# Optimization experiments

Measured on AMD Instinct MI355X. Metric: run time of the kernel, lower is better.

## Reference

```python
import jax, jax.numpy as jnp
import numpy as np

B, T, D_EMB, D_QKV = 8, 2048, 1024, 64
SCALE = 1.0 / (D_QKV ** 0.5)


def setup_inputs() -> dict:
    key = jax.random.key(0)
    kx, kq, kk, kv = jax.random.split(key, 4)
    return {
        "x": jax.random.normal(kx, (B, T, D_EMB), dtype=jnp.float32),
        "Wq": jax.random.normal(kq, (D_EMB, D_QKV), dtype=jnp.float32) * 0.02,
        "Wk": jax.random.normal(kk, (D_EMB, D_QKV), dtype=jnp.float32) * 0.02,
        "Wv": jax.random.normal(kv, (D_EMB, D_QKV), dtype=jnp.float32) * 0.02,
    }


def reference(x, Wq, Wk, Wv):
    # x: [B, T, D_emb]; projections to [B, T, D_qkv]
    q = jnp.einsum("bte,ed->btd", x, Wq)
    k = jnp.einsum("bte,ed->btd", x, Wk)
    v = jnp.einsum("bte,ed->btd", x, Wv)
    # scores: [B, T, T], scaled then causally masked
    scores = jnp.einsum("bqd,bkd->bqk", q, k) * SCALE
    t = x.shape[1]
    causal = jnp.tril(jnp.ones((t, t), dtype=bool))
    scores = jnp.where(causal[None, :, :], scores, -jnp.inf)
    attn = jax.nn.softmax(scores, axis=-1)
    return jnp.einsum("bqk,bkd->bqd", attn, v)
```

## Files before the change

kernel.cpp:

```cpp
#include <hip/hip_runtime.h>

typedef float f32x4 __attribute__((ext_vector_type(4)));
typedef __bf16 bf16x8 __attribute__((ext_vector_type(8)));
typedef __bf16 bf16x4 __attribute__((ext_vector_type(4)));

#define T_ 2048
#define DE 1024
#define DQ 64
#define SCALE 0.125f

#define GL16(gp, lp)                                                        \
  __builtin_amdgcn_global_load_lds(                                         \
      (const __attribute__((address_space(1))) void*)(gp),                  \
      (__attribute__((address_space(3))) void*)(lp), 16, 0, 0)

#define WAITVM(N) asm volatile("s_waitcnt vmcnt(" #N ")" ::: "memory")

__global__ __launch_bounds__(256) void kw_pack(
    const float* __restrict__ Wq, const float* __restrict__ Wk,
    const float* __restrict__ Wv, __bf16* __restrict__ Wf)
{
  int tid = blockIdx.x * 256 + threadIdx.x;
  int lane = tid & 63, f = tid >> 6;
  int t = f % 12, kc = f / 12;
  const float* W = (t < 4) ? Wq : ((t < 8) ? Wk : Wv);
  int nl = (t & 3) * 16 + (lane & 15);
  int k0 = kc * 32 + (lane >> 4) * 8;
  bf16x8 v;
#pragma unroll
  for (int j = 0; j < 8; ++j) v[j] = (__bf16)W[(size_t)(k0 + j) * 64 + nl];
  *(bf16x8*)(Wf + (size_t)tid * 8) = v;
}

__global__ __launch_bounds__(256) void kproj(
    const float* __restrict__ x, const __bf16* __restrict__ Wf,
    __bf16* __restrict__ Qb, __bf16* __restrict__ Kb, __bf16* __restrict__ Vt)
{
  __shared__ char lds[3 * 8192 + 2 * 24576];
  const int tid = threadIdx.x;
  const int lane = tid & 63;
  const int w = tid >> 6;
  const int col = lane & 15, g = lane >> 4;
  const int msub = w & 1;
  const int ng = w >> 1;
  const int mbase = blockIdx.x * 32;

  size_t gsrcA[2];
  int ldstA[2];
#pragma unroll
  for (int cc = 0; cc < 2; ++cc) {
    int q = w * 2 + cc;
    int row = q * 4 + (lane >> 4);
    int kbyte = ((lane & 15) * 16) ^ ((row & 7) << 4);
    gsrcA[cc] = (size_t)(mbase + row) * 4096 + (size_t)kbyte;
    ldstA[cc] = q * 1024 + lane * 16;
  }
  int ofsB[6];
#pragma unroll
  for (int cc = 0; cc < 6; ++cc) ofsB[cc] = (w * 6 + cc) * 1024 + lane * 16;

  f32x4 acc[6];
#pragma unroll
  for (int i = 0; i < 6; ++i) acc[i] = (f32x4){0.f, 0.f, 0.f, 0.f};

  const char* xb = (const char*)x;
  const char* wb = (const char*)Wf;

#define STAGE_A(ks)                                                         \
  {                                                                         \
    char* lb = &lds[((ks) % 3) * 8192];                                     \
    _Pragma("unroll")                                                       \
    for (int cc = 0; cc < 2; ++cc)                                          \
      GL16(xb + gsrcA[cc] + (size_t)(ks) * 256, lb + ldstA[cc]);            \
  }
#define STAGE_B(ks)                                                         \
  {                                                                         \
    char* lb = &lds[24576 + ((ks) & 1) * 24576];                            \
    _Pragma("unroll")                                                       \
    for (int cc = 0; cc < 6; ++cc)                                          \
      GL16(wb + (size_t)(ks) * 24576 + ofsB[cc], lb + ofsB[cc]);            \
  }
#define KSTEP(ks)                                                           \
  {                                                                         \
    const char* la = &lds[((ks) % 3) * 8192];                               \
    const char* lbB = &lds[24576 + ((ks) & 1) * 24576];                     \
    const int arow = msub * 16 + col;                                       \
    const char* abase = la + arow * 256;                                    \
    const int sw = (arow & 7) << 4;                                         \
    _Pragma("unroll")                                                       \
    for (int kh = 0; kh < 2; ++kh) {                                        \
      int kb = kh * 128 + g * 32;                                           \
      f32x4 a0 = *(const f32x4*)(abase + (kb ^ sw));                        \
      f32x4 a1 = *(const f32x4*)(abase + ((kb + 16) ^ sw));                 \
      bf16x8 af;                                                            \
      _Pragma("unroll")                                                     \
      for (int j = 0; j < 4; ++j) { af[j] = (__bf16)a0[j]; af[4 + j] = (__bf16)a1[j]; } \
      _Pragma("unroll")                                                     \
      for (int ii = 0; ii < 6; ++ii) {                                      \
        int nt = ng * 6 + ii;                                               \
        bf16x8 bfr = *(const bf16x8*)(lbB + ((kh * 12 + nt) * 64 + lane) * 16); \
        acc[ii] = __builtin_amdgcn_mfma_f32_16x16x32_bf16(af, bfr, acc[ii], 0, 0, 0); \
      }                                                                     \
    }                                                                       \
  }
#define ITER(ks, vm, doB, doA)                                              \
  WAITVM(vm);                                                               \
  __builtin_amdgcn_s_barrier();                                             \
  __builtin_amdgcn_sched_barrier(0);                                        \
  if (doB) STAGE_B((ks) + 1);                                               \
  if (doA) STAGE_A((ks) + 2);                                               \
  KSTEP(ks);

  STAGE_A(0);
  STAGE_B(0);
  STAGE_A(1);

  ITER(0, 2, 1, 1)  ITER(1, 2, 1, 1)  ITER(2, 2, 1, 1)  ITER(3, 2, 1, 1)
  ITER(4, 2, 1, 1)  ITER(5, 2, 1, 1)  ITER(6, 2, 1, 1)  ITER(7, 2, 1, 1)
  ITER(8, 2, 1, 1)  ITER(9, 2, 1, 1)  ITER(10, 2, 1, 1) ITER(11, 2, 1, 1)
  ITER(12, 2, 1, 1) ITER(13, 2, 1, 1) ITER(14, 2, 1, 0) ITER(15, 0, 0, 0)

#undef ITER
#undef KSTEP
#undef STAGE_B
#undef STAGE_A

  const int b = mbase >> 11;
  const int mrow = mbase + msub * 16 + g * 4;
  const int trow = (mbase & 2047) + msub * 16 + g * 4;
#pragma unroll
  for (int ii = 0; ii < 6; ++ii) {
    int ti = ng * 6 + ii;
    if (ti < 8) {
      __bf16* dst = (ti < 4) ? Qb : Kb;
      int c = (ti & 3) * 16 + col;
#pragma unroll
      for (int r = 0; r < 4; ++r)
        dst[(size_t)(mrow + r) * DQ + c] = (__bf16)acc[ii][r];
    } else {
      int d = (ti - 8) * 16 + col;
      bf16x4 v;
#pragma unroll
      for (int r = 0; r < 4; ++r) v[r] = (__bf16)acc[ii][r];
      *(bf16x4*)(Vt + ((size_t)(b * DQ + d)) * T_ + trow) = v;
    }
  }
}

__global__ __launch_bounds__(256) void kattn(
    const __bf16* __restrict__ Qb, const __bf16* __restrict__ Kb,
    const __bf16* __restrict__ Vt, float* __restrict__ out)
{
  __shared__ char smem[84992];
  const int tid = threadIdx.x;
  const int lane = tid & 63;
  const int w = tid >> 6;
  const int col = lane & 15, g = lane >> 4;
  const int b = blockIdx.x & 7;
  const int jq = 63 - (blockIdx.x >> 3);
  const int qbase = jq * 32;

  char* kbuf = smem + w * 16384;
  char* vbuf = kbuf + 8192;
  __bf16* pld = (__bf16*)(smem + 65536 + w * 4608);
  float* mls = (float*)(smem + 83968);

  bf16x8 qa[2][2];
#pragma unroll
  for (int mt = 0; mt < 2; ++mt) {
    const __bf16* Qp = Qb + (size_t)(b * T_ + qbase + mt * 16 + col) * DQ + g * 8;
    qa[mt][0] = *(const bf16x8*)(Qp);
    qa[mt][1] = *(const bf16x8*)(Qp + 32);
  }

  const char* Kbb = (const char*)(Kb + (size_t)b * T_ * DQ);
  const char* Vbb = (const char*)(Vt + (size_t)b * DQ * T_);

  size_t gofK[8], gofV[8];
  int lof[8];
#pragma unroll
  for (int c = 0; c < 8; ++c) {
    int o = (c * 64 + lane) * 16;
    int row = o >> 7, slot = (o >> 4) & 7;
    int sl = (slot * 16) ^ ((row & 7) << 4);
    lof[c] = o;
    gofK[c] = (size_t)row * 128 + sl;
    gofV[c] = (size_t)row * 4096 + sl;
  }

  f32x4 acc[2][4];
#pragma unroll
  for (int mt = 0; mt < 2; ++mt)
#pragma unroll
    for (int dt = 0; dt < 4; ++dt) acc[mt][dt] = (f32x4){0.f,0.f,0.f,0.f};
  float mrun[2][4], lsum[2][4];
#pragma unroll
  for (int mt = 0; mt < 2; ++mt)
#pragma unroll
    for (int r = 0; r < 4; ++r) { mrun[mt][r] = -1e30f; lsum[mt][r] = 0.f; }

  const int nb = (jq >> 1) + 1;

  if (w < nb) {
    const char* ksrc = Kbb + (size_t)(w * 64) * 128;
    const char* vsrc = Vbb + (size_t)(w * 64) * 2;
#pragma unroll
    for (int c = 0; c < 8; ++c) GL16(ksrc + gofK[c], kbuf + lof[c]);
#pragma unroll
    for (int c = 0; c < 8; ++c) GL16(vsrc + gofV[c], vbuf + lof[c]);
  }

  for (int it = w; it < nb; it += 4) {
    const int nbase = it * 64;

    WAITVM(0);
    __builtin_amdgcn_sched_barrier(0);

    bf16x8 kf_[4][2], vf[4][2];
#pragma unroll
    for (int nt = 0; nt < 4; ++nt)
#pragma unroll
      for (int h = 0; h < 2; ++h) {
        int krow = nt * 16 + col;
        int bo = krow * 128 + ((h * 64 + g * 16) ^ ((krow & 7) << 4));
        kf_[nt][h] = *(const bf16x8*)(kbuf + bo);
        vf[nt][h]  = *(const bf16x8*)(vbuf + bo);
      }
    asm volatile("s_waitcnt lgkmcnt(0)" ::: "memory");
    __builtin_amdgcn_sched_barrier(0);

    if (it + 4 < nb) {
      const char* ksrc = Kbb + (size_t)((it + 4) * 64) * 128;
      const char* vsrc = Vbb + (size_t)((it + 4) * 64) * 2;
#pragma unroll
      for (int c = 0; c < 8; ++c) GL16(ksrc + gofK[c], kbuf + lof[c]);
#pragma unroll
      for (int c = 0; c < 8; ++c) GL16(vsrc + gofV[c], vbuf + lof[c]);
    }
    __builtin_amdgcn_sched_barrier(0);

    f32x4 s[2][4];
#pragma unroll
    for (int mt = 0; mt < 2; ++mt)
#pragma unroll
      for (int nt = 0; nt < 4; ++nt) {
        f32x4 t = __builtin_amdgcn_mfma_f32_16x16x32_bf16(qa[mt][0], kf_[nt][0],
                                                          (f32x4){0.f,0.f,0.f,0.f}, 0, 0, 0);
        s[mt][nt] = __builtin_amdgcn_mfma_f32_16x16x32_bf16(qa[mt][1], kf_[nt][1], t, 0, 0, 0);
      }

#pragma unroll
    for (int mt = 0; mt < 2; ++mt)
#pragma unroll
      for (int nt = 0; nt < 4; ++nt)
#pragma unroll
        for (int r = 0; r < 4; ++r) s[mt][nt][r] *= SCALE;
    if (it == nb - 1) {
#pragma unroll
      for (int mt = 0; mt < 2; ++mt)
#pragma unroll
        for (int nt = 0; nt < 4; ++nt)
#pragma unroll
          for (int r = 0; r < 4; ++r)
            if (nbase + nt * 16 + col > qbase + mt * 16 + g * 4 + r) s[mt][nt][r] = -1e30f;
    }

    float pmax[2][4];
#pragma unroll
    for (int mt = 0; mt < 2; ++mt)
#pragma unroll
      for (int r = 0; r < 4; ++r)
        pmax[mt][r] = fmaxf(fmaxf(s[mt][0][r], s[mt][1][r]), fmaxf(s[mt][2][r], s[mt][3][r]));
    bool need = false;
#pragma unroll
    for (int mt = 0; mt < 2; ++mt)
#pragma unroll
      for (int r = 0; r < 4; ++r)
        need = need || (pmax[mt][r] > mrun[mt][r] + 8.f);

    if (__any(need)) {
      float mv[2][4];
#pragma unroll
      for (int mt = 0; mt < 2; ++mt)
#pragma unroll
        for (int r = 0; r < 4; ++r) mv[mt][r] = pmax[mt][r];
#pragma unroll
      for (int sh = 1; sh <= 8; sh <<= 1)
#pragma unroll
        for (int mt = 0; mt < 2; ++mt)
#pragma unroll
          for (int r = 0; r < 4; ++r) mv[mt][r] = fmaxf(mv[mt][r], __shfl_xor(mv[mt][r], sh, 64));
#pragma unroll
      for (int mt = 0; mt < 2; ++mt)
#pragma unroll
        for (int r = 0; r < 4; ++r) {
          float mn = fmaxf(mrun[mt][r], mv[mt][r]);
          float rs = __expf(mrun[mt][r] - mn);
          mrun[mt][r] = mn;
          float ps = 0.f;
#pragma unroll
          for (int nt = 0; nt < 4; ++nt) {
            s[mt][nt][r] = __expf(s[mt][nt][r] - mn);
            ps += s[mt][nt][r];
          }
          lsum[mt][r] = lsum[mt][r] * rs + ps;
#pragma unroll
          for (int dt = 0; dt < 4; ++dt) acc[mt][dt][r] *= rs;
        }
    } else {
#pragma unroll
      for (int mt = 0; mt < 2; ++mt)
#pragma unroll
        for (int r = 0; r < 4; ++r) {
          float ps = 0.f;
#pragma unroll
          for (int nt = 0; nt < 4; ++nt) {
            s[mt][nt][r] = __expf(s[mt][nt][r] - mrun[mt][r]);
            ps += s[mt][nt][r];
          }
          lsum[mt][r] += ps;
        }
    }

#pragma unroll
    for (int mt = 0; mt < 2; ++mt)
#pragma unroll
      for (int nt = 0; nt < 4; ++nt)
#pragma unroll
        for (int r = 0; r < 4; ++r)
          pld[(mt * 16 + g * 4 + r) * 72 + nt * 16 + col] = (__bf16)s[mt][nt][r];

    bf16x8 pa[2][2];
#pragma unroll
    for (int mt = 0; mt < 2; ++mt) {
      pa[mt][0] = *(const bf16x8*)&pld[(mt * 16 + col) * 72 + g * 8];
      pa[mt][1] = *(const bf16x8*)&pld[(mt * 16 + col) * 72 + 32 + g * 8];
    }

#pragma unroll
    for (int mt = 0; mt < 2; ++mt)
#pragma unroll
      for (int dt = 0; dt < 4; ++dt) {
        f32x4 t = __builtin_amdgcn_mfma_f32_16x16x32_bf16(pa[mt][0], vf[dt][0], acc[mt][dt], 0, 0, 0);
        acc[mt][dt] = __builtin_amdgcn_mfma_f32_16x16x32_bf16(pa[mt][1], vf[dt][1], t, 0, 0, 0);
      }
  }

#pragma unroll
  for (int sh = 1; sh <= 8; sh <<= 1)
#pragma unroll
    for (int mt = 0; mt < 2; ++mt)
#pragma unroll
      for (int r = 0; r < 4; ++r) lsum[mt][r] += __shfl_xor(lsum[mt][r], sh, 64);

  float* accw = (float*)(smem + w * 16384);
#pragma unroll
  for (int mt = 0; mt < 2; ++mt)
#pragma unroll
    for (int r = 0; r < 4; ++r) {
      int row = mt * 16 + g * 4 + r;
      accw[row * 68 + col]      = acc[mt][0][r];
      accw[row * 68 + col + 16] = acc[mt][1][r];
      accw[row * 68 + col + 32] = acc[mt][2][r];
      accw[row * 68 + col + 48] = acc[mt][3][r];
      if (col == 0) { mls[(w * 2 + 0) * 32 + row] = mrun[mt][r]; mls[(w * 2 + 1) * 32 + row] = lsum[mt][r]; }
    }
  __syncthreads();

#pragma unroll
  for (int pass = 0; pass < 2; ++pass) {
    int row = pass * 16 + (tid >> 4);
    int c4 = (tid & 15) * 4;
    float m0 = mls[0 * 32 + row], m1 = mls[2 * 32 + row];
    float m2 = mls[4 * 32 + row], m3 = mls[6 * 32 + row];
    float M = fmaxf(fmaxf(m0, m1), fmaxf(m2, m3));
    float s0 = __expf(m0 - M), s1 = __expf(m1 - M);
    float s2 = __expf(m2 - M), s3 = __expf(m3 - M);
    float L = s0 * mls[1 * 32 + row] + s1 * mls[3 * 32 + row]
            + s2 * mls[5 * 32 + row] + s3 * mls[7 * 32 + row];
    f32x4 a0 = *(const f32x4*)((float*)(smem + 0 * 16384) + row * 68 + c4);
    f32x4 a1 = *(const f32x4*)((float*)(smem + 1 * 16384) + row * 68 + c4);
    f32x4 a2 = *(const f32x4*)((float*)(smem + 2 * 16384) + row * 68 + c4);
    f32x4 a3 = *(const f32x4*)((float*)(smem + 3 * 16384) + row * 68 + c4);
    float inv = 1.f / L;
    f32x4 o;
#pragma unroll
    for (int j = 0; j < 4; ++j)
      o[j] = (s0 * a0[j] + s1 * a1[j] + s2 * a2[j] + s3 * a3[j]) * inv;
    *(f32x4*)(out + (size_t)(b * T_ + qbase + row) * DQ + c4) = o;
  }
}

extern "C" void kernel_launch(void* const* d_in, const int* in_sizes, int n_in,
                              void* d_out, int out_size, void* d_ws, size_t ws_size,
                              hipStream_t stream)
{
  const float* x  = (const float*)d_in[0];
  const float* Wq = (const float*)d_in[1];
  const float* Wk = (const float*)d_in[2];
  const float* Wv = (const float*)d_in[3];
  float* out = (float*)d_out;

  char* ws = (char*)d_ws;
  __bf16* Wf = (__bf16*)(ws);
  __bf16* Qb = (__bf16*)(ws + 0x80000);
  __bf16* Kb = (__bf16*)(ws + 0x80000 + 0x200000);
  __bf16* Vt = (__bf16*)(ws + 0x80000 + 0x400000);

  kw_pack<<<96, 256, 0, stream>>>(Wq, Wk, Wv, Wf);
  kproj<<<512, 256, 0, stream>>>(x, Wf, Qb, Kb, Vt);
  kattn<<<512, 256, 0, stream>>>(Qb, Kb, Vt, out);
}
```

Measured before the change: 46.86 us.

## Enlarge projection tile to 64 rows and reuse weight fragments across four M-fragments

The projection kernel now handles 64 rows of x per block instead of 32, and each wave owns 3 of the 12 output N-tiles across all four 16-row M-fragments. Each B fragment loaded from LDS is reused for four MFMAs, and the whole-block weight staging is amortised over twice as many rows. The cost is a grid of 256 blocks instead of 512 on a 256-CU part, more accumulator registers, a larger LDS footprint (~96KB) that limits occupancy, and deeper outstanding-load waits.

```diff
diff --git a/kernel.cpp b/kernel.cpp
--- a/kernel.cpp
+++ b/kernel.cpp
@@ -36,20 +36,19 @@
     const float* __restrict__ x, const __bf16* __restrict__ Wf,
     __bf16* __restrict__ Qb, __bf16* __restrict__ Kb, __bf16* __restrict__ Vt)
 {
-  __shared__ char lds[3 * 8192 + 2 * 24576];
+  __shared__ char lds[3 * 16384 + 2 * 24576];
   const int tid = threadIdx.x;
   const int lane = tid & 63;
   const int w = tid >> 6;
   const int col = lane & 15, g = lane >> 4;
-  const int msub = w & 1;
-  const int ng = w >> 1;
-  const int mbase = blockIdx.x * 32;
-
-  size_t gsrcA[2];
-  int ldstA[2];
-#pragma unroll
-  for (int cc = 0; cc < 2; ++cc) {
-    int q = w * 2 + cc;
+  const int ng6 = w * 3;
+  const int mbase = blockIdx.x * 64;
+
+  size_t gsrcA[4];
+  int ldstA[4];
+#pragma unroll
+  for (int cc = 0; cc < 4; ++cc) {
+    int q = w * 4 + cc;
     int row = q * 4 + (lane >> 4);
     int kbyte = ((lane & 15) * 16) ^ ((row & 7) << 4);
     gsrcA[cc] = (size_t)(mbase + row) * 4096 + (size_t)kbyte;
@@ -59,47 +58,53 @@
 #pragma unroll
   for (int cc = 0; cc < 6; ++cc) ofsB[cc] = (w * 6 + cc) * 1024 + lane * 16;
 
-  f32x4 acc[6];
-#pragma unroll
-  for (int i = 0; i < 6; ++i) acc[i] = (f32x4){0.f, 0.f, 0.f, 0.f};
+  f32x4 acc[4][3];
+#pragma unroll
+  for (int mf = 0; mf < 4; ++mf)
+#pragma unroll
+    for (int ii = 0; ii < 3; ++ii) acc[mf][ii] = (f32x4){0.f, 0.f, 0.f, 0.f};
 
   const char* xb = (const char*)x;
   const char* wb = (const char*)Wf;
 
 #define STAGE_A(ks)                                                         \
   {                                                                         \
-    char* lb = &lds[((ks) % 3) * 8192];                                     \
+    char* lb = &lds[((ks) % 3) * 16384];                                    \
     _Pragma("unroll")                                                       \
-    for (int cc = 0; cc < 2; ++cc)                                          \
+    for (int cc = 0; cc < 4; ++cc)                                          \
       GL16(xb + gsrcA[cc] + (size_t)(ks) * 256, lb + ldstA[cc]);            \
   }
 #define STAGE_B(ks)                                                         \
   {                                                                         \
-    char* lb = &lds[24576 + ((ks) & 1) * 24576];                            \
+    char* lb = &lds[49152 + ((ks) & 1) * 24576];                            \
     _Pragma("unroll")                                                       \
     for (int cc = 0; cc < 6; ++cc)                                          \
       GL16(wb + (size_t)(ks) * 24576 + ofsB[cc], lb + ofsB[cc]);            \
   }
 #define KSTEP(ks)                                                           \
   {                                                                         \
-    const char* la = &lds[((ks) % 3) * 8192];                               \
-    const char* lbB = &lds[24576 + ((ks) & 1) * 24576];                     \
-    const int arow = msub * 16 + col;                                       \
-    const char* abase = la + arow * 256;                                    \
-    const int sw = (arow & 7) << 4;                                         \
+    const char* la = &lds[((ks) % 3) * 16384];                              \
+    const char* lbB = &lds[49152 + ((ks) & 1) * 24576];                     \
     _Pragma("unroll")                                                       \
     for (int kh = 0; kh < 2; ++kh) {                                        \
-      int kb = kh * 128 + g * 32;                                           \
-      f32x4 a0 = *(const f32x4*)(abase + (kb ^ sw));                        \
-      f32x4 a1 = *(const f32x4*)(abase + ((kb + 16) ^ sw));                 \
-      bf16x8 af;                                                            \
+      bf16x8 af[4];                                                         \
       _Pragma("unroll")                                                     \
-      for (int j = 0; j < 4; ++j) { af[j] = (__bf16)a0[j]; af[4 + j] = (__bf16)a1[j]; } \
+      for (int mf = 0; mf < 4; ++mf) {                                      \
+        const int arow = mf * 16 + col;                                     \
+        const char* abase = la + arow * 256;                                \
+        const int sw = (arow & 7) << 4;                                     \
+        int kb = kh * 128 + g * 32;                                         \
+        f32x4 a0 = *(const f32x4*)(abase + (kb ^ sw));                      \
+        f32x4 a1 = *(const f32x4*)(abase + ((kb + 16) ^ sw));               \
+        _Pragma("unroll")                                                   \
+        for (int j = 0; j < 4; ++j) { af[mf][j] = (__bf16)a0[j]; af[mf][4 + j] = (__bf16)a1[j]; } \
+      }                                                                     \
       _Pragma("unroll")                                                     \
-      for (int ii = 0; ii < 6; ++ii) {                                      \
-        int nt = ng * 6 + ii;                                               \
-        bf16x8 bfr = *(const bf16x8*)(lbB + ((kh * 12 + nt) * 64 + lane) * 16); \
-        acc[ii] = __builtin_amdgcn_mfma_f32_16x16x32_bf16(af, bfr, acc[ii], 0, 0, 0); \
+      for (int ii = 0; ii < 3; ++ii) {                                      \
+        bf16x8 bfr = *(const bf16x8*)(lbB + ((kh * 12 + ng6 + ii) * 64 + lane) * 16); \
+        _Pragma("unroll")                                                   \
+        for (int mf = 0; mf < 4; ++mf)                                      \
+          acc[mf][ii] = __builtin_amdgcn_mfma_f32_16x16x32_bf16(af[mf], bfr, acc[mf][ii], 0, 0, 0); \
       }                                                                     \
     }                                                                       \
   }
@@ -115,10 +120,10 @@
   STAGE_B(0);
   STAGE_A(1);
 
-  ITER(0, 2, 1, 1)  ITER(1, 2, 1, 1)  ITER(2, 2, 1, 1)  ITER(3, 2, 1, 1)
-  ITER(4, 2, 1, 1)  ITER(5, 2, 1, 1)  ITER(6, 2, 1, 1)  ITER(7, 2, 1, 1)
-  ITER(8, 2, 1, 1)  ITER(9, 2, 1, 1)  ITER(10, 2, 1, 1) ITER(11, 2, 1, 1)
-  ITER(12, 2, 1, 1) ITER(13, 2, 1, 1) ITER(14, 2, 1, 0) ITER(15, 0, 0, 0)
+  ITER(0, 4, 1, 1)  ITER(1, 4, 1, 1)  ITER(2, 4, 1, 1)  ITER(3, 4, 1, 1)
+  ITER(4, 4, 1, 1)  ITER(5, 4, 1, 1)  ITER(6, 4, 1, 1)  ITER(7, 4, 1, 1)
+  ITER(8, 4, 1, 1)  ITER(9, 4, 1, 1)  ITER(10, 4, 1, 1) ITER(11, 4, 1, 1)
+  ITER(12, 4, 1, 1) ITER(13, 4, 1, 1) ITER(14, 4, 1, 0) ITER(15, 0, 0, 0)
 
 #undef ITER
 #undef KSTEP
@@ -126,23 +131,26 @@
 #undef STAGE_A
 
   const int b = mbase >> 11;
-  const int mrow = mbase + msub * 16 + g * 4;
-  const int trow = (mbase & 2047) + msub * 16 + g * 4;
-#pragma unroll
-  for (int ii = 0; ii < 6; ++ii) {
-    int ti = ng * 6 + ii;
-    if (ti < 8) {
-      __bf16* dst = (ti < 4) ? Qb : Kb;
-      int c = (ti & 3) * 16 + col;
-#pragma unroll
-      for (int r = 0; r < 4; ++r)
-        dst[(size_t)(mrow + r) * DQ + c] = (__bf16)acc[ii][r];
-    } else {
-      int d = (ti - 8) * 16 + col;
-      bf16x4 v;
-#pragma unroll
-      for (int r = 0; r < 4; ++r) v[r] = (__bf16)acc[ii][r];
-      *(bf16x4*)(Vt + ((size_t)(b * DQ + d)) * T_ + trow) = v;
+#pragma unroll
+  for (int mf = 0; mf < 4; ++mf) {
+    const int mrow = mbase + mf * 16 + g * 4;
+    const int trow = (mbase & 2047) + mf * 16 + g * 4;
+#pragma unroll
+    for (int ii = 0; ii < 3; ++ii) {
+      int ti = ng6 + ii;
+      if (ti < 8) {
+        __bf16* dst = (ti < 4) ? Qb : Kb;
+        int c = (ti & 3) * 16 + col;
+#pragma unroll
+        for (int r = 0; r < 4; ++r)
+          dst[(size_t)(mrow + r) * DQ + c] = (__bf16)acc[mf][ii][r];
+      } else {
+        int d = (ti - 8) * 16 + col;
+        bf16x4 v;
+#pragma unroll
+        for (int r = 0; r < 4; ++r) v[r] = (__bf16)acc[mf][ii][r];
+        *(bf16x4*)(Vt + ((size_t)(b * DQ + d)) * T_ + trow) = v;
+      }
     }
   }
 }
@@ -408,6 +416,6 @@
   __bf16* Vt = (__bf16*)(ws + 0x80000 + 0x400000);
 
   kw_pack<<<96, 256, 0, stream>>>(Wq, Wk, Wv, Wf);
-  kproj<<<512, 256, 0, stream>>>(x, Wf, Qb, Kb, Vt);
+  kproj<<<256, 256, 0, stream>>>(x, Wf, Qb, Kb, Vt);
   kattn<<<512, 256, 0, stream>>>(Qb, Kb, Vt, out);
 }
```

After: 47.48 us. About the same (+1.3%).

## Give each projection warp a private LDS slab to drop block barriers

Applied to the files above, without the earlier changes.

The projection kernel's shared A/B tiles, loaded cooperatively and synchronised with block-wide s_barrier each k-step, are replaced by per-wave private LDS slabs. Each wave loads its own 16 rows of x and its 6 weight tiles, then double-buffers them: it reads fragments to registers, issues the next step's async loads into the other buffer, and runs the MFMAs. This removes all block barriers in the k-loop. The cost is duplicated global loads: the x rows are fetched by two waves and the weight tiles per wave group, and LDS use grows to 128KB per block, which may reduce occupancy.

```diff
diff --git a/kernel.cpp b/kernel.cpp
--- a/kernel.cpp
+++ b/kernel.cpp
@@ -15,6 +15,7 @@
       (__attribute__((address_space(3))) void*)(lp), 16, 0, 0)
 
 #define WAITVM(N) asm volatile("s_waitcnt vmcnt(" #N ")" ::: "memory")
+#define SB __builtin_amdgcn_sched_barrier(0)
 
 __global__ __launch_bounds__(256) void kw_pack(
     const float* __restrict__ Wq, const float* __restrict__ Wk,
@@ -36,7 +37,7 @@
     const float* __restrict__ x, const __bf16* __restrict__ Wf,
     __bf16* __restrict__ Qb, __bf16* __restrict__ Kb, __bf16* __restrict__ Vt)
 {
-  __shared__ char lds[3 * 8192 + 2 * 24576];
+  __shared__ char lds[4][32768];
   const int tid = threadIdx.x;
   const int lane = tid & 63;
   const int w = tid >> 6;
@@ -45,19 +46,27 @@
   const int ng = w >> 1;
   const int mbase = blockIdx.x * 32;
 
-  size_t gsrcA[2];
-  int ldstA[2];
-#pragma unroll
-  for (int cc = 0; cc < 2; ++cc) {
-    int q = w * 2 + cc;
-    int row = q * 4 + (lane >> 4);
-    int kbyte = ((lane & 15) * 16) ^ ((row & 7) << 4);
-    gsrcA[cc] = (size_t)(mbase + row) * 4096 + (size_t)kbyte;
-    ldstA[cc] = q * 1024 + lane * 16;
-  }
-  int ofsB[6];
-#pragma unroll
-  for (int cc = 0; cc < 6; ++cc) ofsB[cc] = (w * 6 + cc) * 1024 + lane * 16;
+  char* slab = &lds[w][0];
+
+  size_t gsrcA[4];
+  int ldstA[4];
+#pragma unroll
+  for (int cc = 0; cc < 4; ++cc) {
+    int slot = cc * 64 + lane;
+    int row = slot >> 4, s16 = slot & 15;
+    int kbyte = (s16 * 16) ^ ((row & 7) << 4);
+    gsrcA[cc] = (size_t)(mbase + msub * 16 + row) * 4096 + (size_t)kbyte;
+    ldstA[cc] = slot * 16;
+  }
+  size_t gofB[12];
+  int ldstB[12];
+#pragma unroll
+  for (int cc = 0; cc < 12; ++cc) {
+    int kh = cc / 6, ii = cc % 6;
+    int jj = kh * 12 + ng * 6 + ii;
+    gofB[cc] = (size_t)jj * 1024 + (size_t)lane * 16;
+    ldstB[cc] = cc * 1024 + lane * 16;
+  }
 
   f32x4 acc[6];
 #pragma unroll
@@ -65,65 +74,62 @@
 
   const char* xb = (const char*)x;
   const char* wb = (const char*)Wf;
-
-#define STAGE_A(ks)                                                         \
-  {                                                                         \
-    char* lb = &lds[((ks) % 3) * 8192];                                     \
-    _Pragma("unroll")                                                       \
-    for (int cc = 0; cc < 2; ++cc)                                          \
-      GL16(xb + gsrcA[cc] + (size_t)(ks) * 256, lb + ldstA[cc]);            \
-  }
-#define STAGE_B(ks)                                                         \
-  {                                                                         \
-    char* lb = &lds[24576 + ((ks) & 1) * 24576];                            \
-    _Pragma("unroll")                                                       \
-    for (int cc = 0; cc < 6; ++cc)                                          \
-      GL16(wb + (size_t)(ks) * 24576 + ofsB[cc], lb + ofsB[cc]);            \
-  }
-#define KSTEP(ks)                                                           \
-  {                                                                         \
-    const char* la = &lds[((ks) % 3) * 8192];                               \
-    const char* lbB = &lds[24576 + ((ks) & 1) * 24576];                     \
-    const int arow = msub * 16 + col;                                       \
-    const char* abase = la + arow * 256;                                    \
-    const int sw = (arow & 7) << 4;                                         \
-    _Pragma("unroll")                                                       \
-    for (int kh = 0; kh < 2; ++kh) {                                        \
-      int kb = kh * 128 + g * 32;                                           \
-      f32x4 a0 = *(const f32x4*)(abase + (kb ^ sw));                        \
-      f32x4 a1 = *(const f32x4*)(abase + ((kb + 16) ^ sw));                 \
-      bf16x8 af;                                                            \
-      _Pragma("unroll")                                                     \
-      for (int j = 0; j < 4; ++j) { af[j] = (__bf16)a0[j]; af[4 + j] = (__bf16)a1[j]; } \
-      _Pragma("unroll")                                                     \
-      for (int ii = 0; ii < 6; ++ii) {                                      \
-        int nt = ng * 6 + ii;                                               \
-        bf16x8 bfr = *(const bf16x8*)(lbB + ((kh * 12 + nt) * 64 + lane) * 16); \
-        acc[ii] = __builtin_amdgcn_mfma_f32_16x16x32_bf16(af, bfr, acc[ii], 0, 0, 0); \
-      }                                                                     \
-    }                                                                       \
-  }
-#define ITER(ks, vm, doB, doA)                                              \
-  WAITVM(vm);                                                               \
-  __builtin_amdgcn_s_barrier();                                             \
-  __builtin_amdgcn_sched_barrier(0);                                        \
-  if (doB) STAGE_B((ks) + 1);                                               \
-  if (doA) STAGE_A((ks) + 2);                                               \
-  KSTEP(ks);
-
-  STAGE_A(0);
-  STAGE_B(0);
-  STAGE_A(1);
-
-  ITER(0, 2, 1, 1)  ITER(1, 2, 1, 1)  ITER(2, 2, 1, 1)  ITER(3, 2, 1, 1)
-  ITER(4, 2, 1, 1)  ITER(5, 2, 1, 1)  ITER(6, 2, 1, 1)  ITER(7, 2, 1, 1)
-  ITER(8, 2, 1, 1)  ITER(9, 2, 1, 1)  ITER(10, 2, 1, 1) ITER(11, 2, 1, 1)
-  ITER(12, 2, 1, 1) ITER(13, 2, 1, 1) ITER(14, 2, 1, 0) ITER(15, 0, 0, 0)
-
-#undef ITER
-#undef KSTEP
-#undef STAGE_B
-#undef STAGE_A
+  const int sw = (col & 7) << 4;
+
+  {
+    char* ab = slab;
+    char* bb = slab + 8192;
+#pragma unroll
+    for (int cc = 0; cc < 4; ++cc)  GL16(xb + gsrcA[cc], ab + ldstA[cc]);
+#pragma unroll
+    for (int cc = 0; cc < 12; ++cc) GL16(wb + gofB[cc], bb + ldstB[cc]);
+  }
+
+#pragma unroll
+  for (int ks = 0; ks < 16; ++ks) {
+    const int p = ks & 1;
+    const char* ab = slab + p * 4096;
+    const char* bb = slab + 8192 + p * 12288;
+
+    WAITVM(0);
+    SB;
+
+    f32x4 a0[2], a1[2];
+    bf16x8 bfr[2][6];
+#pragma unroll
+    for (int kh = 0; kh < 2; ++kh) {
+      int kb = kh * 128 + g * 32;
+      a0[kh] = *(const f32x4*)(ab + col * 256 + (kb ^ sw));
+      a1[kh] = *(const f32x4*)(ab + col * 256 + ((kb + 16) ^ sw));
+#pragma unroll
+      for (int ii = 0; ii < 6; ++ii)
+        bfr[kh][ii] = *(const bf16x8*)(bb + ((kh * 6 + ii) * 64 + lane) * 16);
+    }
+    asm volatile("s_waitcnt lgkmcnt(0)" ::: "memory");
+    SB;
+
+    if (ks < 15) {
+      char* ab2 = slab + (p ^ 1) * 4096;
+      char* bb2 = slab + 8192 + (p ^ 1) * 12288;
+#pragma unroll
+      for (int cc = 0; cc < 4; ++cc)
+        GL16(xb + gsrcA[cc] + (size_t)(ks + 1) * 256, ab2 + ldstA[cc]);
+#pragma unroll
+      for (int cc = 0; cc < 12; ++cc)
+        GL16(wb + (size_t)(ks + 1) * 24576 + gofB[cc], bb2 + ldstB[cc]);
+    }
+    SB;
+
+#pragma unroll
+    for (int kh = 0; kh < 2; ++kh) {
+      bf16x8 af;
+#pragma unroll
+      for (int j = 0; j < 4; ++j) { af[j] = (__bf16)a0[kh][j]; af[4 + j] = (__bf16)a1[kh][j]; }
+#pragma unroll
+      for (int ii = 0; ii < 6; ++ii)
+        acc[ii] = __builtin_amdgcn_mfma_f32_16x16x32_bf16(af, bfr[kh][ii], acc[ii], 0, 0, 0);
+    }
+  }
 
   const int b = mbase >> 11;
   const int mrow = mbase + msub * 16 + g * 4;
@@ -214,7 +220,7 @@
     const int nbase = it * 64;
 
     WAITVM(0);
-    __builtin_amdgcn_sched_barrier(0);
+    SB;
 
     bf16x8 kf_[4][2], vf[4][2];
 #pragma unroll
@@ -227,7 +233,7 @@
         vf[nt][h]  = *(const bf16x8*)(vbuf + bo);
       }
     asm volatile("s_waitcnt lgkmcnt(0)" ::: "memory");
-    __builtin_amdgcn_sched_barrier(0);
+    SB;
 
     if (it + 4 < nb) {
       const char* ksrc = Kbb + (size_t)((it + 4) * 64) * 128;
@@ -237,7 +243,7 @@
 #pragma unroll
       for (int c = 0; c < 8; ++c) GL16(vsrc + gofV[c], vbuf + lof[c]);
     }
-    __builtin_amdgcn_sched_barrier(0);
+    SB;
 
     f32x4 s[2][4];
 #pragma unroll
```

New measurement: 58.75 us. +25.4%, slower.
